# Kernel tuning notes

Measured on AMD Instinct MI355X. Metric: run time of the kernel, lower is better.

Reference implementation:

```python
import jax, jax.numpy as jnp
import numpy as np

SEQ, BATCH, EMBED = 2048, 4, 768
NUM_HEADS = 12
HEAD_DIM = EMBED // NUM_HEADS
SCALING = HEAD_DIM ** -0.5


def setup_inputs() -> dict:
    key = jax.random.key(0)
    ks = jax.random.split(key, 9)
    std = 0.02
    d = {"x": jax.random.normal(ks[0], (SEQ, BATCH, EMBED), dtype=jnp.float32)}
    for i, n in enumerate(["q", "k", "v", "out"]):
        d[f"W{n}"] = jax.random.normal(ks[1 + 2 * i], (EMBED, EMBED), dtype=jnp.float32) * std
        d[f"b{n}"] = jax.random.normal(ks[2 + 2 * i], (EMBED,), dtype=jnp.float32) * std
    return d


def reference(x, Wq, bq, Wk, bk, Wv, bv, Wout, bout):
    # x: [tgt_len, bsz, embed_dim] (fairseq seq-first layout per forward body)
    T, B, E = x.shape
    H, Dh = NUM_HEADS, HEAD_DIM

    q = (x @ Wq.T + bq) * SCALING          # [T, B, E]
    k = x @ Wk.T + bk
    v = x @ Wv.T + bv

    # view(T, B*H, Dh).transpose(0, 1) -> [B*H, T, Dh]
    q = q.reshape(T, B * H, Dh).transpose(1, 0, 2)
    k = k.reshape(T, B * H, Dh).transpose(1, 0, 2)
    v = v.reshape(T, B * H, Dh).transpose(1, 0, 2)

    # bmm: [B*H, T, T] attention scores (full O(T^2) matrix, as in the original)
    scores = jnp.einsum('bqd,bkd->bqk', q, k)
    # util_softmax with onnx_trace=True: softmax in float32, then cast back
    probs = jax.nn.softmax(scores.astype(jnp.float32), axis=-1).astype(scores.dtype)
    # dropout p=0.0 -> identity

    attn = jnp.einsum('bqk,bkd->bqd', probs, v)           # [B*H, T, Dh]
    attn = attn.transpose(1, 0, 2).reshape(T, B, E)       # [T, B, E]
    return attn @ Wout.T + bout
```

## Files before the change

### kernel.cpp

```cpp
#include <hip/hip_runtime.h>
#include <hip/hip_bf16.h>

#define SEQ 2048
#define BATCH 4
#define EMBED 768
#define NHEAD 12
#define HDIM 64
#define NROWS (SEQ*BATCH)
#define GH (BATCH*NHEAD)
#define KVBLK 64
#define KVHALF (SEQ/2)

typedef __bf16 bf16;
typedef __attribute__((ext_vector_type(4))) __bf16 bf16x4;
typedef __attribute__((ext_vector_type(8))) __bf16 bf16x8;
typedef __attribute__((ext_vector_type(4))) float f32x4;
typedef __attribute__((ext_vector_type(16))) float f32x16;
typedef __attribute__((ext_vector_type(2))) unsigned uint2v;
typedef __attribute__((ext_vector_type(4))) unsigned uint4v;

#define LOG2E 1.44269504088896340736f

__global__ __launch_bounds__(256) void cvt_kernel(const float* __restrict__ in,
                                                  bf16* __restrict__ out, int n4) {
  int i = blockIdx.x * 256 + threadIdx.x;
  if (i >= n4) return;
  float4 v = reinterpret_cast<const float4*>(in)[i];
  bf16x4 o;
  o[0] = (bf16)v.x; o[1] = (bf16)v.y; o[2] = (bf16)v.z; o[3] = (bf16)v.w;
  reinterpret_cast<bf16x4*>(out)[i] = o;
}

__global__ __launch_bounds__(256) void cvt_w4(const float* __restrict__ Wq,
                                              const float* __restrict__ Wk,
                                              const float* __restrict__ Wv,
                                              const float* __restrict__ Wo,
                                              bf16* __restrict__ Wqkvb,
                                              bf16* __restrict__ Wob) {
  const int n4 = EMBED * EMBED / 4;
  int i = blockIdx.x * 256 + threadIdx.x;
  if (i >= n4) return;
  const float* src;
  bf16* dst;
  switch (blockIdx.y) {
    case 0: src = Wq; dst = Wqkvb; break;
    case 1: src = Wk; dst = Wqkvb + EMBED * EMBED; break;
    case 2: src = Wv; dst = Wqkvb + 2 * EMBED * EMBED; break;
    default: src = Wo; dst = Wob; break;
  }
  float4 v = reinterpret_cast<const float4*>(src)[i];
  bf16x4 o;
  o[0] = (bf16)v.x; o[1] = (bf16)v.y; o[2] = (bf16)v.z; o[3] = (bf16)v.w;
  reinterpret_cast<bf16x4*>(dst)[i] = o;
}

__global__ __launch_bounds__(256) void gemm_qkv(const bf16* __restrict__ A,
                                                const bf16* __restrict__ B,
                                                const float* __restrict__ bq,
                                                const float* __restrict__ bk,
                                                const float* __restrict__ bv,
                                                bf16* __restrict__ Qh,
                                                bf16* __restrict__ Kh,
                                                bf16* __restrict__ Vt) {
  constexpr int K = EMBED;
  __shared__ bf16 As[128 * 32];
  __shared__ bf16 Bs[128 * 32];
  const int tid = threadIdx.x;
  const int l = tid & 63;
  const int w = tid >> 6;
  const int row0 = blockIdx.x * 128;
  const int col0 = blockIdx.y * 128;
  const int wm = (w >> 1) * 64;
  const int wn = (w & 1) * 64;
  const int l15 = l & 15, l4 = l >> 4;

  f32x4 acc[4][4] = {};

  for (int k0 = 0; k0 < K; k0 += 32) {
#pragma unroll
    for (int i = 0; i < 2; ++i) {
      int c = tid + i * 256;
      int r = c >> 2, cc = c & 3;
      __builtin_amdgcn_global_load_lds(
          (const __attribute__((address_space(1))) void*)(A + (size_t)(row0 + r) * K + k0 + cc * 8),
          (__attribute__((address_space(3))) void*)(As + c * 8), 16, 0, 0);
    }
#pragma unroll
    for (int i = 0; i < 2; ++i) {
      int c = tid + i * 256;
      int r = c >> 2, cc = c & 3;
      __builtin_amdgcn_global_load_lds(
          (const __attribute__((address_space(1))) void*)(B + (size_t)(col0 + r) * K + k0 + cc * 8),
          (__attribute__((address_space(3))) void*)(Bs + c * 8), 16, 0, 0);
    }
    __syncthreads();

    bf16x8 af[4], bfr[4];
#pragma unroll
    for (int i = 0; i < 4; ++i)
      af[i] = *reinterpret_cast<const bf16x8*>(&As[(wm + i * 16 + l15) * 32 + l4 * 8]);
#pragma unroll
    for (int j = 0; j < 4; ++j)
      bfr[j] = *reinterpret_cast<const bf16x8*>(&Bs[(wn + j * 16 + l15) * 32 + l4 * 8]);
#pragma unroll
    for (int i = 0; i < 4; ++i)
#pragma unroll
      for (int j = 0; j < 4; ++j)
        acc[i][j] = __builtin_amdgcn_mfma_f32_16x16x32_bf16(af[i], bfr[j], acc[i][j], 0, 0, 0);
    __syncthreads();
  }

  const int sel = blockIdx.y / 6;
  const float* bias = sel == 0 ? bq : (sel == 1 ? bk : bv);
  const int colbase = col0 - sel * EMBED;
#pragma unroll
  for (int i = 0; i < 4; ++i) {
#pragma unroll
    for (int j = 0; j < 4; ++j) {
      int col = colbase + wn + j * 16 + l15;
      float bia = bias[col];
#pragma unroll
      for (int r = 0; r < 4; ++r) {
        int row = row0 + wm + i * 16 + l4 * 4 + r;
        float v = acc[i][j][r] + bia;
        int t = row >> 2, bb = row & 3;
        int hh = col >> 6, d = col & 63;
        int g = bb * NHEAD + hh;
        if (sel == 0)      Qh[((size_t)g * SEQ + t) * HDIM + d] = (bf16)(v * (0.125f * LOG2E));
        else if (sel == 1) Kh[((size_t)g * SEQ + t) * HDIM + d] = (bf16)v;
        else               Vt[((size_t)g * HDIM + d) * SEQ + t] = (bf16)v;
      }
    }
  }
}

__global__ __launch_bounds__(256) void gemm_out(const bf16* __restrict__ A,
                                                const bf16* __restrict__ B,
                                                const float* __restrict__ bias,
                                                float* __restrict__ outp) {
  constexpr int K = EMBED;
  __shared__ bf16 As[128 * 32];
  __shared__ bf16 Bs[128 * 32];
  const int tid = threadIdx.x;
  const int l = tid & 63;
  const int w = tid >> 6;
  const int row0 = blockIdx.x * 128;
  const int col0 = blockIdx.y * 128;
  const int wm = (w >> 1) * 64;
  const int wn = (w & 1) * 64;
  const int l15 = l & 15, l4 = l >> 4;

  f32x4 acc[4][4] = {};

  for (int k0 = 0; k0 < K; k0 += 32) {
#pragma unroll
    for (int i = 0; i < 2; ++i) {
      int c = tid + i * 256;
      int r = c >> 2, cc = c & 3;
      __builtin_amdgcn_global_load_lds(
          (const __attribute__((address_space(1))) void*)(A + (size_t)(row0 + r) * K + k0 + cc * 8),
          (__attribute__((address_space(3))) void*)(As + c * 8), 16, 0, 0);
    }
#pragma unroll
    for (int i = 0; i < 2; ++i) {
      int c = tid + i * 256;
      int r = c >> 2, cc = c & 3;
      __builtin_amdgcn_global_load_lds(
          (const __attribute__((address_space(1))) void*)(B + (size_t)(col0 + r) * K + k0 + cc * 8),
          (__attribute__((address_space(3))) void*)(Bs + c * 8), 16, 0, 0);
    }
    __syncthreads();

    bf16x8 af[4], bfr[4];
#pragma unroll
    for (int i = 0; i < 4; ++i)
      af[i] = *reinterpret_cast<const bf16x8*>(&As[(wm + i * 16 + l15) * 32 + l4 * 8]);
#pragma unroll
    for (int j = 0; j < 4; ++j)
      bfr[j] = *reinterpret_cast<const bf16x8*>(&Bs[(wn + j * 16 + l15) * 32 + l4 * 8]);
#pragma unroll
    for (int i = 0; i < 4; ++i)
#pragma unroll
      for (int j = 0; j < 4; ++j)
        acc[i][j] = __builtin_amdgcn_mfma_f32_16x16x32_bf16(af[i], bfr[j], acc[i][j], 0, 0, 0);
    __syncthreads();
  }

#pragma unroll
  for (int i = 0; i < 4; ++i) {
#pragma unroll
    for (int j = 0; j < 4; ++j) {
      int col = col0 + wn + j * 16 + l15;
      float bia = bias[col];
#pragma unroll
      for (int r = 0; r < 4; ++r) {
        int row = row0 + wm + i * 16 + l4 * 4 + r;
        outp[(size_t)row * EMBED + col] = acc[i][j][r] + bia;
      }
    }
  }
}

__global__ __launch_bounds__(256, 4) void attn_kernel(const bf16* __restrict__ Qh,
                                                      const bf16* __restrict__ Kh,
                                                      const bf16* __restrict__ Vt,
                                                      bf16* __restrict__ O0,
                                                      bf16* __restrict__ O1,
                                                      float* __restrict__ Sums) {
  const int g = blockIdx.x % GH;
  const int r2 = blockIdx.x / GH;
  const int half = r2 & 1;
  const int q0 = (r2 >> 1) * 128;
  const int kvbase = half * KVHALF;
  const int tid = threadIdx.x;
  const int w = tid >> 6, l = tid & 63;
  const int l31 = l & 31, l5 = l >> 5;
  const int qw = q0 + w * 32;
  const int r7 = l31 & 7;

  __shared__ bf16 Ks[2][KVBLK * HDIM];
  __shared__ bf16 Vs[2][HDIM * KVBLK];

  const bf16* Qp = Qh + (size_t)g * SEQ * HDIM;
  const bf16* Kp = Kh + (size_t)g * SEQ * HDIM;
  const bf16* Vp = Vt + (size_t)g * HDIM * SEQ;

#define STAGE_K(buf, kv0)                                                               \
  do {                                                                                  \
    _Pragma("unroll") for (int i = 0; i < 2; ++i) {                                     \
      int t = i * 256 + tid;                                                            \
      int r_ = t >> 3, c_ = t & 7;                                                      \
      __builtin_amdgcn_global_load_lds(                                                 \
          (const __attribute__((address_space(1))) void*)(Kp + (size_t)((kv0) + r_) * HDIM + ((c_ ^ (r_ & 7)) * 8)), \
          (__attribute__((address_space(3))) void*)(&Ks[buf][t * 8]), 16, 0, 0);        \
    }                                                                                   \
  } while (0)

#define STAGE_V(buf, kv0)                                                               \
  do {                                                                                  \
    _Pragma("unroll") for (int i = 0; i < 2; ++i) {                                     \
      int t = i * 256 + tid;                                                            \
      int r_ = t >> 3, c_ = t & 7;                                                      \
      __builtin_amdgcn_global_load_lds(                                                 \
          (const __attribute__((address_space(1))) void*)(Vp + (size_t)r_ * SEQ + (kv0) + ((c_ ^ (r_ & 7)) * 8)), \
          (__attribute__((address_space(3))) void*)(&Vs[buf][t * 8]), 16, 0, 0);        \
    }                                                                                   \
  } while (0)

  bf16x8 bq[4];
#pragma unroll
  for (int m = 0; m < 4; ++m)
    bq[m] = *reinterpret_cast<const bf16x8*>(
        Qp + (size_t)(qw + l31) * HDIM + m * 16 + l5 * 8);

  f32x16 acco[2] = {};
  float lsum = 0.f;

  STAGE_K(0, kvbase);
  STAGE_V(0, kvbase);
  __syncthreads();

  int cur = 0;
  for (int kv0 = kvbase; kv0 < kvbase + KVHALF; kv0 += KVBLK) {
    int nxt = kvbase + (((kv0 - kvbase) + KVBLK) & (KVHALF - 1));
    STAGE_V(cur ^ 1, nxt);
    STAGE_K(cur ^ 1, nxt);

#pragma unroll
    for (int h = 0; h < 2; ++h) {
      f32x16 s = {};
#pragma unroll
      for (int m = 0; m < 4; ++m) {
        bf16x8 ak = *reinterpret_cast<const bf16x8*>(
            &Ks[cur][(32 * h + l31) * 64 + (((2 * m + l5) ^ r7) * 8)]);
        __builtin_amdgcn_s_setprio(1);
        s = __builtin_amdgcn_mfma_f32_32x32x16_bf16(ak, bq[m], s, 0, 0, 0);
        __builtin_amdgcn_s_setprio(0);
      }

      unsigned pg[8];
#pragma unroll
      for (int gq = 0; gq < 4; ++gq) {
        float p0 = exp2f(s[4 * gq + 0]);
        float p1 = exp2f(s[4 * gq + 1]);
        float p2 = exp2f(s[4 * gq + 2]);
        float p3 = exp2f(s[4 * gq + 3]);
        lsum += (p0 + p1) + (p2 + p3);
        bf16x4 q4;
        q4[0] = (bf16)p0; q4[1] = (bf16)p1; q4[2] = (bf16)p2; q4[3] = (bf16)p3;
        uint2v d2 = __builtin_bit_cast(uint2v, q4);
        pg[2 * gq] = d2[0];
        pg[2 * gq + 1] = d2[1];
      }

#pragma unroll
      for (int j = 0; j < 2; ++j) {
        unsigned sx = l5 ? pg[4 * j + 0] : pg[4 * j + 2];
        unsigned sy = l5 ? pg[4 * j + 1] : pg[4 * j + 3];
        unsigned rx = (unsigned)__shfl_xor((int)sx, 32);
        unsigned ry = (unsigned)__shfl_xor((int)sy, 32);
        unsigned ox = l5 ? pg[4 * j + 2] : pg[4 * j + 0];
        unsigned oy = l5 ? pg[4 * j + 3] : pg[4 * j + 1];
        uint4v f;
        f[0] = l5 ? rx : ox;  f[1] = l5 ? ry : oy;
        f[2] = l5 ? ox : rx;  f[3] = l5 ? oy : ry;
        bf16x8 pb = __builtin_bit_cast(bf16x8, f);
#pragma unroll
        for (int dt = 0; dt < 2; ++dt) {
          bf16x8 av = *reinterpret_cast<const bf16x8*>(
              &Vs[cur][(dt * 32 + l31) * 64 + (((4 * h + 2 * j + l5) ^ r7) * 8)]);
          __builtin_amdgcn_s_setprio(1);
          acco[dt] = __builtin_amdgcn_mfma_f32_32x32x16_bf16(av, pb, acco[dt], 0, 0, 0);
          __builtin_amdgcn_s_setprio(0);
        }
      }
    }
    __syncthreads();
    cur ^= 1;
  }

  float tot = lsum + __shfl_xor(lsum, 32);
  bf16* Op = half ? O1 : O0;
  float* Sp = Sums + (size_t)half * GH * SEQ + (size_t)g * SEQ;
  const int tq = qw + l31;
  if (l5 == 0) Sp[tq] = tot;
  const int bb = g / NHEAD, hh = g % NHEAD;
  const size_t rowbase = ((size_t)tq * BATCH + bb) * EMBED + hh * HDIM;
#pragma unroll
  for (int dt = 0; dt < 2; ++dt)
#pragma unroll
    for (int gq = 0; gq < 4; ++gq) {
      int d = dt * 32 + 8 * gq + 4 * l5;
      bf16x4 o4;
      o4[0] = (bf16)acco[dt][4 * gq + 0];
      o4[1] = (bf16)acco[dt][4 * gq + 1];
      o4[2] = (bf16)acco[dt][4 * gq + 2];
      o4[3] = (bf16)acco[dt][4 * gq + 3];
      *reinterpret_cast<bf16x4*>(Op + rowbase + d) = o4;
    }
}

__global__ __launch_bounds__(256) void attn_combine(const bf16* __restrict__ O0,
                                                    const bf16* __restrict__ O1,
                                                    const float* __restrict__ Sums,
                                                    bf16* __restrict__ attnb) {
  int i = blockIdx.x * 256 + threadIdx.x;
  int flat = i * 8;
  int row = flat / EMBED;
  int e = flat - row * EMBED;
  int tq = row >> 2, bb = row & 3;
  int hh = e >> 6;
  int g = bb * NHEAD + hh;
  float s = Sums[(size_t)g * SEQ + tq] + Sums[(size_t)GH * SEQ + (size_t)g * SEQ + tq];
  float rinv = __builtin_amdgcn_rcpf(s);
  bf16x8 a0 = *reinterpret_cast<const bf16x8*>(O0 + flat);
  bf16x8 a1 = *reinterpret_cast<const bf16x8*>(O1 + flat);
  bf16x8 o;
#pragma unroll
  for (int j = 0; j < 8; ++j)
    o[j] = (bf16)(((float)a0[j] + (float)a1[j]) * rinv);
  *reinterpret_cast<bf16x8*>(attnb + flat) = o;
}

extern "C" void kernel_launch(void* const* d_in, const int* in_sizes, int n_in,
                              void* d_out, int out_size, void* d_ws, size_t ws_size,
                              hipStream_t stream) {
  const float* x  = (const float*)d_in[0];
  const float* Wq = (const float*)d_in[1];
  const float* bq = (const float*)d_in[2];
  const float* Wk = (const float*)d_in[3];
  const float* bk = (const float*)d_in[4];
  const float* Wv = (const float*)d_in[5];
  const float* bv = (const float*)d_in[6];
  const float* Wo = (const float*)d_in[7];
  const float* bo = (const float*)d_in[8];
  float* out = (float*)d_out;

  char* ws = (char*)d_ws;
  bf16* xb    = (bf16*)(ws + 0);
  bf16* Wqkvb = (bf16*)(ws + 12582912);
  bf16* Wob   = (bf16*)(ws + 16121856);
  bf16* Qh    = (bf16*)(ws + 17301504);
  bf16* Kh    = (bf16*)(ws + 29884416);
  bf16* Vt    = (bf16*)(ws + 42467328);
  bf16* attnb = (bf16*)(ws + 55050240);
  float* Sums = (float*)(ws + 67633152);

  cvt_kernel<<<6144, 256, 0, stream>>>(x, xb, NROWS * EMBED / 4);
  cvt_w4<<<dim3(576, 4), 256, 0, stream>>>(Wq, Wk, Wv, Wo, Wqkvb, Wob);

  gemm_qkv<<<dim3(NROWS / 128, 18), 256, 0, stream>>>(xb, Wqkvb, bq, bk, bv, Qh, Kh, Vt);

  attn_kernel<<<GH * (SEQ / 128) * 2, 256, 0, stream>>>(Qh, Kh, Vt, xb, attnb, Sums);
  attn_combine<<<NROWS * EMBED / 8 / 256, 256, 0, stream>>>(xb, attnb, Sums, attnb);

  gemm_out<<<dim3(NROWS / 128, EMBED / 128), 256, 0, stream>>>(attnb, Wob, bo, out);
}
```

Baseline: 180.8 us.

## Drop split-KV attention, compute row sums via MFMA, fuse normalization

Removes the two-way KV split and the separate combine kernel, so each block walks the full key sequence and normalizes its output in-kernel. Softmax row sums are now produced by an extra MFMA against a ones vector instead of per-lane scalar adds. The LDS swizzle is extended to also XOR in row bits 3-4. This halves the grid (768 blocks) and removes the partial-output round trip through memory, at the cost of less parallelism per head and an extra MFMA per PV step.

```diff
diff --git a/kernel.cpp b/kernel.cpp
--- a/kernel.cpp
+++ b/kernel.cpp
@@ -9,7 +9,6 @@
 #define NROWS (SEQ*BATCH)
 #define GH (BATCH*NHEAD)
 #define KVBLK 64
-#define KVHALF (SEQ/2)
 
 typedef __bf16 bf16;
 typedef __attribute__((ext_vector_type(4))) __bf16 bf16x4;
@@ -201,22 +200,18 @@
   }
 }
 
+#define SWZ(r) ((((r) & 7) ^ (((r) >> 3) & 3)))
 __global__ __launch_bounds__(256, 4) void attn_kernel(const bf16* __restrict__ Qh,
                                                       const bf16* __restrict__ Kh,
                                                       const bf16* __restrict__ Vt,
-                                                      bf16* __restrict__ O0,
-                                                      bf16* __restrict__ O1,
-                                                      float* __restrict__ Sums) {
+                                                      bf16* __restrict__ attnb) {
   const int g = blockIdx.x % GH;
-  const int r2 = blockIdx.x / GH;
-  const int half = r2 & 1;
-  const int q0 = (r2 >> 1) * 128;
-  const int kvbase = half * KVHALF;
+  const int q0 = (blockIdx.x / GH) * 128;
   const int tid = threadIdx.x;
   const int w = tid >> 6, l = tid & 63;
   const int l31 = l & 31, l5 = l >> 5;
   const int qw = q0 + w * 32;
-  const int r7 = l31 & 7;
+  const int rsw = SWZ(l31);
 
   __shared__ bf16 Ks[2][KVBLK * HDIM];
   __shared__ bf16 Vs[2][HDIM * KVBLK];
@@ -231,7 +226,7 @@
       int t = i * 256 + tid;                                                            \
       int r_ = t >> 3, c_ = t & 7;                                                      \
       __builtin_amdgcn_global_load_lds(                                                 \
-          (const __attribute__((address_space(1))) void*)(Kp + (size_t)((kv0) + r_) * HDIM + ((c_ ^ (r_ & 7)) * 8)), \
+          (const __attribute__((address_space(1))) void*)(Kp + (size_t)((kv0) + r_) * HDIM + ((c_ ^ SWZ(r_)) * 8)), \
           (__attribute__((address_space(3))) void*)(&Ks[buf][t * 8]), 16, 0, 0);        \
     }                                                                                   \
   } while (0)
@@ -242,7 +237,7 @@
       int t = i * 256 + tid;                                                            \
       int r_ = t >> 3, c_ = t & 7;                                                      \
       __builtin_amdgcn_global_load_lds(                                                 \
-          (const __attribute__((address_space(1))) void*)(Vp + (size_t)r_ * SEQ + (kv0) + ((c_ ^ (r_ & 7)) * 8)), \
+          (const __attribute__((address_space(1))) void*)(Vp + (size_t)r_ * SEQ + (kv0) + ((c_ ^ SWZ(r_)) * 8)), \
           (__attribute__((address_space(3))) void*)(&Vs[buf][t * 8]), 16, 0, 0);        \
     }                                                                                   \
   } while (0)
@@ -253,16 +248,20 @@
     bq[m] = *reinterpret_cast<const bf16x8*>(
         Qp + (size_t)(qw + l31) * HDIM + m * 16 + l5 * 8);
 
+  bf16x8 vone;
+#pragma unroll
+  for (int i = 0; i < 8; ++i) vone[i] = (bf16)1.0f;
+
   f32x16 acco[2] = {};
-  float lsum = 0.f;
-
-  STAGE_K(0, kvbase);
-  STAGE_V(0, kvbase);
+  f32x16 accs = {};
+
+  STAGE_K(0, 0);
+  STAGE_V(0, 0);
   __syncthreads();
 
   int cur = 0;
-  for (int kv0 = kvbase; kv0 < kvbase + KVHALF; kv0 += KVBLK) {
-    int nxt = kvbase + (((kv0 - kvbase) + KVBLK) & (KVHALF - 1));
+  for (int kv0 = 0; kv0 < SEQ; kv0 += KVBLK) {
+    int nxt = (kv0 + KVBLK) & (SEQ - 1);
     STAGE_V(cur ^ 1, nxt);
     STAGE_K(cur ^ 1, nxt);
 
@@ -272,7 +271,7 @@
 #pragma unroll
       for (int m = 0; m < 4; ++m) {
         bf16x8 ak = *reinterpret_cast<const bf16x8*>(
-            &Ks[cur][(32 * h + l31) * 64 + (((2 * m + l5) ^ r7) * 8)]);
+            &Ks[cur][(32 * h + l31) * 64 + (((2 * m + l5) ^ rsw) * 8)]);
         __builtin_amdgcn_s_setprio(1);
         s = __builtin_amdgcn_mfma_f32_32x32x16_bf16(ak, bq[m], s, 0, 0, 0);
         __builtin_amdgcn_s_setprio(0);
@@ -285,7 +284,6 @@
         float p1 = exp2f(s[4 * gq + 1]);
         float p2 = exp2f(s[4 * gq + 2]);
         float p3 = exp2f(s[4 * gq + 3]);
-        lsum += (p0 + p1) + (p2 + p3);
         bf16x4 q4;
         q4[0] = (bf16)p0; q4[1] = (bf16)p1; q4[2] = (bf16)p2; q4[3] = (bf16)p3;
         uint2v d2 = __builtin_bit_cast(uint2v, q4);
@@ -308,22 +306,22 @@
 #pragma unroll
         for (int dt = 0; dt < 2; ++dt) {
           bf16x8 av = *reinterpret_cast<const bf16x8*>(
-              &Vs[cur][(dt * 32 + l31) * 64 + (((4 * h + 2 * j + l5) ^ r7) * 8)]);
+              &Vs[cur][(dt * 32 + l31) * 64 + (((4 * h + 2 * j + l5) ^ rsw) * 8)]);
           __builtin_amdgcn_s_setprio(1);
           acco[dt] = __builtin_amdgcn_mfma_f32_32x32x16_bf16(av, pb, acco[dt], 0, 0, 0);
           __builtin_amdgcn_s_setprio(0);
         }
+        __builtin_amdgcn_s_setprio(1);
+        accs = __builtin_amdgcn_mfma_f32_32x32x16_bf16(vone, pb, accs, 0, 0, 0);
+        __builtin_amdgcn_s_setprio(0);
       }
     }
     __syncthreads();
     cur ^= 1;
   }
 
-  float tot = lsum + __shfl_xor(lsum, 32);
-  bf16* Op = half ? O1 : O0;
-  float* Sp = Sums + (size_t)half * GH * SEQ + (size_t)g * SEQ;
+  const float rinv = __builtin_amdgcn_rcpf(accs[0]);
   const int tq = qw + l31;
-  if (l5 == 0) Sp[tq] = tot;
   const int bb = g / NHEAD, hh = g % NHEAD;
   const size_t rowbase = ((size_t)tq * BATCH + bb) * EMBED + hh * HDIM;
 #pragma unroll
@@ -332,34 +330,12 @@
     for (int gq = 0; gq < 4; ++gq) {
       int d = dt * 32 + 8 * gq + 4 * l5;
       bf16x4 o4;
-      o4[0] = (bf16)acco[dt][4 * gq + 0];
-      o4[1] = (bf16)acco[dt][4 * gq + 1];
-      o4[2] = (bf16)acco[dt][4 * gq + 2];
-      o4[3] = (bf16)acco[dt][4 * gq + 3];
-      *reinterpret_cast<bf16x4*>(Op + rowbase + d) = o4;
-    }
-}
-
-__global__ __launch_bounds__(256) void attn_combine(const bf16* __restrict__ O0,
-                                                    const bf16* __restrict__ O1,
-                                                    const float* __restrict__ Sums,
-                                                    bf16* __restrict__ attnb) {
-  int i = blockIdx.x * 256 + threadIdx.x;
-  int flat = i * 8;
-  int row = flat / EMBED;
-  int e = flat - row * EMBED;
-  int tq = row >> 2, bb = row & 3;
-  int hh = e >> 6;
-  int g = bb * NHEAD + hh;
-  float s = Sums[(size_t)g * SEQ + tq] + Sums[(size_t)GH * SEQ + (size_t)g * SEQ + tq];
-  float rinv = __builtin_amdgcn_rcpf(s);
-  bf16x8 a0 = *reinterpret_cast<const bf16x8*>(O0 + flat);
-  bf16x8 a1 = *reinterpret_cast<const bf16x8*>(O1 + flat);
-  bf16x8 o;
-#pragma unroll
-  for (int j = 0; j < 8; ++j)
-    o[j] = (bf16)(((float)a0[j] + (float)a1[j]) * rinv);
-  *reinterpret_cast<bf16x8*>(attnb + flat) = o;
+      o4[0] = (bf16)(acco[dt][4 * gq + 0] * rinv);
+      o4[1] = (bf16)(acco[dt][4 * gq + 1] * rinv);
+      o4[2] = (bf16)(acco[dt][4 * gq + 2] * rinv);
+      o4[3] = (bf16)(acco[dt][4 * gq + 3] * rinv);
+      *reinterpret_cast<bf16x4*>(attnb + rowbase + d) = o4;
+    }
 }
 
 extern "C" void kernel_launch(void* const* d_in, const int* in_sizes, int n_in,
@@ -384,15 +360,13 @@
   bf16* Kh    = (bf16*)(ws + 29884416);
   bf16* Vt    = (bf16*)(ws + 42467328);
   bf16* attnb = (bf16*)(ws + 55050240);
-  float* Sums = (float*)(ws + 67633152);
 
   cvt_kernel<<<6144, 256, 0, stream>>>(x, xb, NROWS * EMBED / 4);
   cvt_w4<<<dim3(576, 4), 256, 0, stream>>>(Wq, Wk, Wv, Wo, Wqkvb, Wob);
 
   gemm_qkv<<<dim3(NROWS / 128, 18), 256, 0, stream>>>(xb, Wqkvb, bq, bk, bv, Qh, Kh, Vt);
 
-  attn_kernel<<<GH * (SEQ / 128) * 2, 256, 0, stream>>>(Qh, Kh, Vt, xb, attnb, Sums);
-  attn_combine<<<NROWS * EMBED / 8 / 256, 256, 0, stream>>>(xb, attnb, Sums, attnb);
+  attn_kernel<<<GH * (SEQ / 128), 256, 0, stream>>>(Qh, Kh, Vt, attnb);
 
   gemm_out<<<dim3(NROWS / 128, EMBED / 128), 256, 0, stream>>>(attnb, Wob, bo, out);
 }
```

Measured after the change: 175.2 us. 3.1% less time.
